# Kernel tuning notes

Hardware: AMD Instinct MI355X
Metric: run time of the kernel (lower is better)

## Reference

```python
import jax, jax.numpy as jnp
import numpy as np

K = 3
IN_C = 64
OUT_C = 64
EMB = 16
N_NODES = 2048
BATCH = 64


def avwgcn(X, E, weights_pool, bias_pool):
    # X: [B, N, C], E: [N, D], weights_pool: [D, K, C, O], bias_pool: [D, O]
    N = E.shape[0]
    A = jax.nn.softmax(jax.nn.relu(E @ E.T), axis=1)  # [N, N]
    supports = [jnp.eye(N, dtype=X.dtype), A]
    for _ in range(2, K):  # Chebyshev recursion
        supports.append(2.0 * (A @ supports[-1]) - supports[-2])
    S = jnp.stack(supports, axis=0)  # [K, N, N]
    W = jnp.einsum('nd,dkio->nkio', E, weights_pool)  # [N, K, C, O]
    b = E @ bias_pool  # [N, O]
    XG = jnp.einsum('knm,bmc->bnkc', S, X)  # [B, N, K, C]
    return jnp.einsum('bnki,nkio->bno', XG, W) + b  # [B, N, O]


def glorot(key, shape):
    fan = shape[-2] + shape[-1]
    std = jnp.sqrt(2.0 / fan)
    return jax.random.normal(key, shape, dtype=jnp.float32) * std


def setup_inputs() -> dict:
    key = jax.random.key(0)
    ks = jax.random.split(key, 6)
    cat_c = IN_C + OUT_C
    return {
        'X': jax.random.normal(ks[0], (BATCH, N_NODES, IN_C), dtype=jnp.float32),
        'E': jax.random.normal(ks[1], (N_NODES, EMB), dtype=jnp.float32),
        'H': jax.random.normal(ks[2], (BATCH, N_NODES, OUT_C), dtype=jnp.float32),
        'gate_weights_pool': glorot(ks[3], (EMB, K, cat_c, 2 * OUT_C)),
        'gate_bias_pool': jnp.zeros((EMB, 2 * OUT_C), dtype=jnp.float32),
        'update_weights_pool': glorot(ks[4], (EMB, K, cat_c, OUT_C)),
        'update_bias_pool': jnp.zeros((EMB, OUT_C), dtype=jnp.float32),
    }


def reference(X, E, H, gate_weights_pool, gate_bias_pool, update_weights_pool, update_bias_pool):
    XH = jnp.concatenate([X, H], axis=-1)  # [B, N, in+out]
    ZR = jax.nn.sigmoid(avwgcn(XH, E, gate_weights_pool, gate_bias_pool))
    Z, R = jnp.split(ZR, 2, axis=-1)
    C = jnp.concatenate([X, Z * H], axis=-1)
    HC = jnp.tanh(avwgcn(C, E, update_weights_pool, update_bias_pool))
    return R * H + (1.0 - R) * HC
```

## Files before the change

kernel.cpp:

```cpp
#include <hip/hip_runtime.h>
#include <hip/hip_fp16.h>


#define B_  64
#define N_  2048
#define D_  16
#define CO_ 64
#define CC_ 128

typedef _Float16 f16x8 __attribute__((ext_vector_type(8)));
typedef float    f32x4 __attribute__((ext_vector_type(4)));

static __device__ __forceinline__ uint pack2(float a, float b) {
  return (uint)__half_as_ushort(__float2half(a)) |
         ((uint)__half_as_ushort(__float2half(b)) << 16);
}

__global__ __launch_bounds__(256)
void k_softmaxA(const float* __restrict__ E, __half* __restrict__ A) {
  const int n = blockIdx.x, t = threadIdx.x;
  __shared__ float row[N_];
  __shared__ float red[4];
  const float4* en4 = reinterpret_cast<const float4*>(E + n * D_);
  const float4 e0 = en4[0], e1 = en4[1], e2 = en4[2], e3 = en4[3];
  float lmax = 0.f;
  for (int m = t; m < N_; m += 256) {
    const float4* em4 = reinterpret_cast<const float4*>(E + m * D_);
    const float4 f0 = em4[0], f1 = em4[1], f2 = em4[2], f3 = em4[3];
    float d = e0.x*f0.x + e0.y*f0.y + e0.z*f0.z + e0.w*f0.w
            + e1.x*f1.x + e1.y*f1.y + e1.z*f1.z + e1.w*f1.w
            + e2.x*f2.x + e2.y*f2.y + e2.z*f2.z + e2.w*f2.w
            + e3.x*f3.x + e3.y*f3.y + e3.z*f3.z + e3.w*f3.w;
    d = fmaxf(d, 0.f);
    row[m] = d;
    lmax = fmaxf(lmax, d);
  }
  #pragma unroll
  for (int off = 32; off > 0; off >>= 1) lmax = fmaxf(lmax, __shfl_down(lmax, off));
  __syncthreads();
  if ((t & 63) == 0) red[t >> 6] = lmax;
  __syncthreads();
  const float gmax = fmaxf(fmaxf(red[0], red[1]), fmaxf(red[2], red[3]));
  float lsum = 0.f;
  for (int m = t; m < N_; m += 256) {
    float v = __expf(row[m] - gmax);
    row[m] = v;
    lsum += v;
  }
  #pragma unroll
  for (int off = 32; off > 0; off >>= 1) lsum += __shfl_down(lsum, off);
  __syncthreads();
  if ((t & 63) == 0) red[t >> 6] = lsum;
  __syncthreads();
  const float rinv = 1.f / (red[0] + red[1] + red[2] + red[3]);
  for (int m = t; m < N_; m += 256)
    A[(long)n * N_ + m] = __float2half(row[m] * rinv);
}

__global__ __launch_bounds__(256)
void k_gemm(const __half* __restrict__ Ag, const __half* __restrict__ Bg,
            __half* __restrict__ Cg, int K, int lda, int ldb, int ldc,
            long sB, long sC) {
  const int m0 = blockIdx.x * 128;
  const int n0 = blockIdx.y * 128;
  Bg += (long)blockIdx.z * sB;
  Cg += (long)blockIdx.z * sC;
  __shared__ __half As[128][40];
  __shared__ __half Bs[128][40];
  const int t = threadIdx.x, lane = t & 63, wid = t >> 6;
  const int wm = (wid & 1) * 64, wn = (wid >> 1) * 64;
  f32x4 acc[4][4] = {};
  const int ar = t >> 1, aseg = t & 1;
  const int bc = t & 127, bkg = (t >> 7) * 8;

  for (int kt = 0; kt < K; kt += 32) {
    {
      const uint4* asrc = reinterpret_cast<const uint4*>(
          Ag + (long)(m0 + ar) * lda + kt + aseg * 16);
      uint4 av0 = asrc[0], av1 = asrc[1];
      *reinterpret_cast<uint4*>(&As[ar][aseg * 16])     = av0;
      *reinterpret_cast<uint4*>(&As[ar][aseg * 16 + 8]) = av1;
    }
    #pragma unroll
    for (int it = 0; it < 2; ++it) {
      const int kk = bkg + it * 16;
      const __half* bsrc = Bg + (long)(kt + kk) * ldb + n0 + bc;
      ushort h[8];
      #pragma unroll
      for (int j = 0; j < 8; ++j) h[j] = __half_as_ushort(bsrc[(long)j * ldb]);
      uint4 pk;
      pk.x = (uint)h[0] | ((uint)h[1] << 16);
      pk.y = (uint)h[2] | ((uint)h[3] << 16);
      pk.z = (uint)h[4] | ((uint)h[5] << 16);
      pk.w = (uint)h[6] | ((uint)h[7] << 16);
      *reinterpret_cast<uint4*>(&Bs[bc][kk]) = pk;
    }
    __syncthreads();
    f16x8 af[4], bf[4];
    #pragma unroll
    for (int i = 0; i < 4; ++i) {
      af[i] = *reinterpret_cast<const f16x8*>(&As[wm + i * 16 + (lane & 15)][(lane >> 4) * 8]);
      bf[i] = *reinterpret_cast<const f16x8*>(&Bs[wn + i * 16 + (lane & 15)][(lane >> 4) * 8]);
    }
    #pragma unroll
    for (int i = 0; i < 4; ++i)
      #pragma unroll
      for (int j = 0; j < 4; ++j)
        acc[i][j] = __builtin_amdgcn_mfma_f32_16x16x32_f16(af[i], bf[j], acc[i][j], 0, 0, 0);
    __syncthreads();
  }
  const int cr = (lane >> 4) * 4, ccol = lane & 15;
  #pragma unroll
  for (int i = 0; i < 4; ++i)
    #pragma unroll
    for (int j = 0; j < 4; ++j) {
      const int gr = m0 + wm + i * 16 + cr;
      const int gc = n0 + wn + j * 16 + ccol;
      #pragma unroll
      for (int r = 0; r < 4; ++r)
        Cg[(long)(gr + r) * ldc + gc] = __float2half(acc[i][j][r]);
    }
}

template <int OSZ>
__global__ __launch_bounds__(256)
void k_wpre(const float* __restrict__ pool, const float* __restrict__ E,
            __half* __restrict__ W, int n0) {
  const int WC = 3 * OSZ * 128;
  const int col0 = blockIdx.x * 512;
  const int kc = col0 / (OSZ * 128);
  const int o0 = (col0 - kc * OSZ * 128) >> 7;
  const int t = threadIdx.x;
  __shared__ float PoolS[16 * 768];
  __shared__ float Es[32][16];
  for (int p = t; p < 512; p += 256)
    Es[p >> 4][p & 15] = E[(n0 + blockIdx.y * 32 + (p >> 4)) * 16 + (p & 15)];
  for (int p = t; p < 16 * 512; p += 256) {
    const int d = p >> 9, jl = p & 511;
    const int o = o0 + (jl >> 7), i = jl & 127;
    PoolS[d * 768 + (jl >> 3) * 12 + (jl & 7)] =
        pool[((long)(d * 3 + kc) * 128 + i) * OSZ + o];
  }
  __syncthreads();
  const int c8 = (t & 63) * 8;
  const int r0 = (t >> 6) * 8;
  const int cbase = (t & 63) * 12;
  float acc[8][8] = {};
  #pragma unroll
  for (int d = 0; d < 16; ++d) {
    const float4 pv0 = *reinterpret_cast<const float4*>(&PoolS[d * 768 + cbase]);
    const float4 pv1 = *reinterpret_cast<const float4*>(&PoolS[d * 768 + cbase + 4]);
    #pragma unroll
    for (int rr = 0; rr < 8; ++rr) {
      const float e = Es[r0 + rr][d];
      acc[rr][0] += e * pv0.x; acc[rr][1] += e * pv0.y;
      acc[rr][2] += e * pv0.z; acc[rr][3] += e * pv0.w;
      acc[rr][4] += e * pv1.x; acc[rr][5] += e * pv1.y;
      acc[rr][6] += e * pv1.z; acc[rr][7] += e * pv1.w;
    }
  }
  #pragma unroll
  for (int rr = 0; rr < 8; ++rr) {
    const int nloc = blockIdx.y * 32 + r0 + rr;
    uint4 pk;
    pk.x = pack2(acc[rr][0], acc[rr][1]);
    pk.y = pack2(acc[rr][2], acc[rr][3]);
    pk.z = pack2(acc[rr][4], acc[rr][5]);
    pk.w = pack2(acc[rr][6], acc[rr][7]);
    *reinterpret_cast<uint4*>(W + (long)nloc * WC + col0 + c8) = pk;
  }
}

__global__ __launch_bounds__(256)
void k_build_xh(const float* __restrict__ X, const float* __restrict__ H,
                __half* __restrict__ XH) {
  const long i = (long)blockIdx.x * 256 + threadIdx.x;
  const long bn = i >> 5;
  const int  q  = (int)(i & 31);
  const float* src = (q < 16 ? X : H) + bn * 64 + (q & 15) * 4;
  const float4 v = *reinterpret_cast<const float4*>(src);
  ushort4 h;
  h.x = __half_as_ushort(__float2half(v.x));
  h.y = __half_as_ushort(__float2half(v.y));
  h.z = __half_as_ushort(__float2half(v.z));
  h.w = __half_as_ushort(__float2half(v.w));
  *reinterpret_cast<ushort4*>(XH + bn * CC_ + q * 4) = h;
}

__global__ __launch_bounds__(256)
void k_cast_f16(const float* __restrict__ src, __half* __restrict__ dst, int nquads) {
  const int i = blockIdx.x * 256 + threadIdx.x;
  if (i >= nquads) return;
  const float4 v = reinterpret_cast<const float4*>(src)[i];
  ushort4 h;
  h.x = __half_as_ushort(__float2half(v.x));
  h.y = __half_as_ushort(__float2half(v.y));
  h.z = __half_as_ushort(__float2half(v.z));
  h.w = __half_as_ushort(__float2half(v.w));
  *reinterpret_cast<ushort4*>(dst + i * 4) = h;
}

__global__ __launch_bounds__(256)
void k_bias(const float* __restrict__ E, const float* __restrict__ pool,
            float* __restrict__ bias, int O) {
  const int idx = blockIdx.x * 256 + threadIdx.x;
  const int n = idx / O, o = idx - n * O;
  float s = 0.f;
  #pragma unroll
  for (int d = 0; d < D_; ++d) s += E[n * D_ + d] * pool[d * O + o];
  bias[idx] = s;
}

static __device__ __forceinline__
void stage_data(int kc, const __half* XH, const __half* G1, const __half* G2,
                long base, int b, int seg, __half (*Ds)[136]) {
  if (kc < 2) {
    const uint4* s = reinterpret_cast<const uint4*>((kc ? G1 : XH) + base);
    uint4 v0 = s[0], v1 = s[1], v2 = s[2], v3 = s[3];
    uint4* d = reinterpret_cast<uint4*>(&Ds[b][seg * 32]);
    d[0] = v0; d[1] = v1; d[2] = v2; d[3] = v3;
  } else {
    const uint4* sg = reinterpret_cast<const uint4*>(G2 + base);
    const uint4* sx = reinterpret_cast<const uint4*>(XH + base);
    #pragma unroll
    for (int q = 0; q < 4; ++q) {
      uint4 g = sg[q], x = sx[q], r;
      const __half2* gh = reinterpret_cast<const __half2*>(&g);
      const __half2* xh = reinterpret_cast<const __half2*>(&x);
      __half2* rh = reinterpret_cast<__half2*>(&r);
      #pragma unroll
      for (int w = 0; w < 4; ++w) rh[w] = __hsub2(__hadd2(gh[w], gh[w]), xh[w]);
      reinterpret_cast<uint4*>(&Ds[b][seg * 32])[q] = r;
    }
  }
}

template <bool PRE>
__global__ __launch_bounds__(256)
void k_gate(const __half* __restrict__ XH, const __half* __restrict__ G1,
            const __half* __restrict__ G2, const __half* __restrict__ Wsrc,
            const float* __restrict__ E, const float* __restrict__ bg,
            const float* __restrict__ H, __half* __restrict__ XHw,
            __half* __restrict__ R, int n0) {
  const int bl = blockIdx.x, n = n0 + bl;
  const int t = threadIdx.x, lane = t & 63, wid = t >> 6;
  __shared__ __half Ws[128][136];
  __shared__ __half Ds[64][136];
  __shared__ float es[D_];
  if constexpr (!PRE) {
    if (t < D_) es[t] = E[n * D_ + t];
    __syncthreads();
  }
  f32x4 acc[4][2] = {};
  #pragma unroll
  for (int kc = 0; kc < 3; ++kc) {
    {
      const int b = t & 63, seg = t >> 6;
      stage_data(kc, XH, G1, G2, ((long)b * N_ + n) * CC_ + seg * 32, b, seg, Ds);
    }
    if constexpr (PRE) {
      const uint4* s4 = reinterpret_cast<const uint4*>(
          Wsrc + ((long)(bl * 3 + kc) * 128 + (t >> 1)) * 128 + (t & 1) * 64);
      uint4* dst = reinterpret_cast<uint4*>(&Ws[t >> 1][(t & 1) * 64]);
      #pragma unroll
      for (int q = 0; q < 8; ++q) dst[q] = s4[q];
    } else {
      const __half* pk = Wsrc + (long)kc * 128 * 128;
      for (int p = t; p < 64 * 128; p += 256) {
        const int o2 = p & 63, i = p >> 6;
        float w0 = 0.f, w1 = 0.f;
        #pragma unroll
        for (int d = 0; d < D_; ++d) {
          const __half2 h2 = *reinterpret_cast<const __half2*>(
              pk + (long)d * 3 * 128 * 128 + i * 128 + o2 * 2);
          const float e = es[d];
          w0 += e * __half2float(h2.x);
          w1 += e * __half2float(h2.y);
        }
        Ws[o2 * 2][i]     = __float2half(w0);
        Ws[o2 * 2 + 1][i] = __float2half(w1);
      }
    }
    __syncthreads();
    #pragma unroll
    for (int ks = 0; ks < 4; ++ks) {
      f16x8 a[4], bf[2];
      #pragma unroll
      for (int i = 0; i < 4; ++i)
        a[i] = *reinterpret_cast<const f16x8*>(&Ds[i * 16 + (lane & 15)][ks * 32 + (lane >> 4) * 8]);
      #pragma unroll
      for (int j = 0; j < 2; ++j)
        bf[j] = *reinterpret_cast<const f16x8*>(&Ws[wid * 32 + j * 16 + (lane & 15)][ks * 32 + (lane >> 4) * 8]);
      #pragma unroll
      for (int i = 0; i < 4; ++i)
        #pragma unroll
        for (int j = 0; j < 2; ++j)
          acc[i][j] = __builtin_amdgcn_mfma_f32_16x16x32_f16(a[i], bf[j], acc[i][j], 0, 0, 0);
    }
    __syncthreads();
  }
  const int cr = (lane >> 4) * 4, co = lane & 15;
  #pragma unroll
  for (int i = 0; i < 4; ++i)
    #pragma unroll
    for (int j = 0; j < 2; ++j) {
      const int o = wid * 32 + j * 16 + co;
      const float bv = bg[n * 128 + o];
      #pragma unroll
      for (int r = 0; r < 4; ++r) {
        const int b = i * 16 + cr + r;
        const float v = acc[i][j][r] + bv;
        const float s = 1.f / (1.f + __expf(-v));
        const long base = ((long)b * N_ + n) * CO_ + (o & 63);
        if (o < 64) {
          XHw[((long)b * N_ + n) * CC_ + 64 + o] = __float2half(s * H[base]);
        } else {
          R[base] = __float2half(s);
        }
      }
    }
}

template <bool PRE>
__global__ __launch_bounds__(256)
void k_update(const __half* __restrict__ C, const __half* __restrict__ G1,
              const __half* __restrict__ G2, const __half* __restrict__ Wsrc,
              const float* __restrict__ E, const float* __restrict__ bu,
              const float* __restrict__ H, const __half* __restrict__ R,
              float* __restrict__ out, int n0) {
  const int bl = blockIdx.x, n = n0 + bl;
  const int t = threadIdx.x, lane = t & 63, wid = t >> 6;
  __shared__ __half Ws[64][136];
  __shared__ __half Ds[64][136];
  __shared__ float es[D_];
  if constexpr (!PRE) {
    if (t < D_) es[t] = E[n * D_ + t];
    __syncthreads();
  }
  f32x4 acc[4] = {};
  #pragma unroll
  for (int kc = 0; kc < 3; ++kc) {
    {
      const int b = t & 63, seg = t >> 6;
      stage_data(kc, C, G1, G2, ((long)b * N_ + n) * CC_ + seg * 32, b, seg, Ds);
    }
    if constexpr (PRE) {
      const uint4* s4 = reinterpret_cast<const uint4*>(
          Wsrc + ((long)(bl * 3 + kc) * 64 + (t >> 2)) * 128 + (t & 3) * 32);
      uint4* dst = reinterpret_cast<uint4*>(&Ws[t >> 2][(t & 3) * 32]);
      #pragma unroll
      for (int q = 0; q < 4; ++q) dst[q] = s4[q];
    } else {
      const __half* pk = Wsrc + (long)kc * 128 * 64;
      for (int p = t; p < 32 * 128; p += 256) {
        const int o2 = p & 31, i = p >> 5;
        float w0 = 0.f, w1 = 0.f;
        #pragma unroll
        for (int d = 0; d < D_; ++d) {
          const __half2 h2 = *reinterpret_cast<const __half2*>(
              pk + (long)d * 3 * 128 * 64 + i * 64 + o2 * 2);
          const float e = es[d];
          w0 += e * __half2float(h2.x);
          w1 += e * __half2float(h2.y);
        }
        Ws[o2 * 2][i]     = __float2half(w0);
        Ws[o2 * 2 + 1][i] = __float2half(w1);
      }
    }
    __syncthreads();
    #pragma unroll
    for (int ks = 0; ks < 4; ++ks) {
      f16x8 a[4], bf;
      #pragma unroll
      for (int i = 0; i < 4; ++i)
        a[i] = *reinterpret_cast<const f16x8*>(&Ds[i * 16 + (lane & 15)][ks * 32 + (lane >> 4) * 8]);
      bf = *reinterpret_cast<const f16x8*>(&Ws[wid * 16 + (lane & 15)][ks * 32 + (lane >> 4) * 8]);
      #pragma unroll
      for (int i = 0; i < 4; ++i)
        acc[i] = __builtin_amdgcn_mfma_f32_16x16x32_f16(a[i], bf, acc[i], 0, 0, 0);
    }
    __syncthreads();
  }
  const int cr = (lane >> 4) * 4, co = lane & 15;
  const int o = wid * 16 + co;
  const float bv = bu[n * 64 + o];
  #pragma unroll
  for (int i = 0; i < 4; ++i)
    #pragma unroll
    for (int r = 0; r < 4; ++r) {
      const int b = i * 16 + cr + r;
      const long idx = ((long)b * N_ + n) * CO_ + o;
      const float hc = tanhf(acc[i][r] + bv);
      const float rr = __half2float(R[idx]);
      out[idx] = rr * H[idx] + (1.f - rr) * hc;
    }
}

extern "C" void kernel_launch(void* const* d_in, const int* in_sizes, int n_in,
                              void* d_out, int out_size, void* d_ws, size_t ws_size,
                              hipStream_t stream) {
  const float* X  = (const float*)d_in[0];
  const float* E  = (const float*)d_in[1];
  const float* H  = (const float*)d_in[2];
  const float* gp = (const float*)d_in[3];
  const float* gb = (const float*)d_in[4];
  const float* up = (const float*)d_in[5];
  const float* ub = (const float*)d_in[6];
  float* out = (float*)d_out;

  size_t off = 0;
  auto alloc = [&](size_t bytes) {
    void* p = (char*)d_ws + off;
    off += (bytes + 255) & ~(size_t)255;
    return p;
  };
  __half* A16  = (__half*)alloc((size_t)N_ * N_ * 2);
  __half* XH   = (__half*)alloc((size_t)B_ * N_ * CC_ * 2);
  __half* G1   = (__half*)alloc((size_t)B_ * N_ * CC_ * 2);
  __half* G2   = (__half*)alloc((size_t)B_ * N_ * CC_ * 2);
  __half* Rb   = (__half*)alloc((size_t)B_ * N_ * CO_ * 2);
  float*  bg   = (float*)alloc((size_t)N_ * 128 * 4);
  float*  bu   = (float*)alloc((size_t)N_ * 64 * 4);

  __half* Wbuf = (__half*)((char*)d_ws + off);
  const size_t rem = (ws_size > off) ? ws_size - off : 0;
  long cgl = (long)(rem / 98304) & ~31L;
  long cul = (long)(rem / 49152) & ~31L;
  const int cg = (int)(cgl > N_ ? N_ : cgl);
  const int cu = (int)(cul > N_ ? N_ : cul);
  const bool pre = cg >= 32;

  const long sXH = (long)N_ * CC_;

  k_bias<<<1024, 256, 0, stream>>>(E, gb, bg, 128);
  k_bias<<<512, 256, 0, stream>>>(E, ub, bu, 64);
  k_softmaxA<<<N_, 256, 0, stream>>>(E, A16);
  k_build_xh<<<16384, 256, 0, stream>>>(X, H, XH);

  k_gemm<<<dim3(16, 1, B_), 256, 0, stream>>>(A16, XH, G1, N_, N_, CC_, CC_, sXH, sXH);
  k_gemm<<<dim3(16, 1, B_), 256, 0, stream>>>(A16, G1, G2, N_, N_, CC_, CC_, sXH, sXH);

  __half* pg = nullptr;
  __half* pu = nullptr;
  if (pre) {
    for (int n0 = 0; n0 < N_; n0 += cg) {
      const int cnt = (N_ - n0 < cg) ? N_ - n0 : cg;
      k_wpre<128><<<dim3(96, cnt / 32), 256, 0, stream>>>(gp, E, Wbuf, n0);
      k_gate<true><<<cnt, 256, 0, stream>>>(XH, G1, G2, Wbuf, E, bg, H, XH, Rb, n0);
    }
  } else {
    pg = (__half*)alloc((size_t)D_ * 3 * 128 * 128 * 2);
    pu = (__half*)alloc((size_t)D_ * 3 * 128 * 64 * 2);
    k_cast_f16<<<768, 256, 0, stream>>>(gp, pg, 196608);
    k_cast_f16<<<384, 256, 0, stream>>>(up, pu, 98304);
    k_gate<false><<<N_, 256, 0, stream>>>(XH, G1, G2, pg, E, bg, H, XH, Rb, 0);
  }

  k_gemm<<<dim3(16, 1, B_), 256, 0, stream>>>(A16, XH, G1, N_, N_, CC_, CC_, sXH, sXH);
  k_gemm<<<dim3(16, 1, B_), 256, 0, stream>>>(A16, G1, G2, N_, N_, CC_, CC_, sXH, sXH);

  if (pre) {
    for (int n0 = 0; n0 < N_; n0 += cu) {
      const int cnt = (N_ - n0 < cu) ? N_ - n0 : cu;
      k_wpre<64><<<dim3(48, cnt / 32), 256, 0, stream>>>(up, E, Wbuf, n0);
      k_update<true><<<cnt, 256, 0, stream>>>(XH, G1, G2, Wbuf, E, bu, H, Rb, out, n0);
    }
  } else {
    k_update<false><<<N_, 256, 0, stream>>>(XH, G1, G2, pu, E, bu, H, Rb, out, 0);
  }
}
```

Baseline: 1.014 ms.

## Rewrite support GEMM with direct global-to-LDS loads, XOR-swizzled tiles, K=64 steps

Replaces the generic fp16 GEMM used for the four A×X support products with a specialized kernel. The A tile is loaded straight into LDS via global_load_lds, and the B tile is read as 16-byte vectors and transposed into an XOR-swizzled LDS layout. Each K step grows from 32 to 64, which halves the number of barriers. The aim is to cut LDS bank conflicts, the scalar strided B loads, and sync overhead. In exchange, dimensions are hardcoded (N_, CC_) and the kernel relies on a low-level builtin.

```diff
diff --git a/kernel.cpp b/kernel.cpp
--- a/kernel.cpp
+++ b/kernel.cpp
@@ -10,6 +10,12 @@
 
 typedef _Float16 f16x8 __attribute__((ext_vector_type(8)));
 typedef float    f32x4 __attribute__((ext_vector_type(4)));
+typedef unsigned short u16x8 __attribute__((ext_vector_type(8)));
+
+#define GLOAD_LDS16(g, l)                                          \
+  __builtin_amdgcn_global_load_lds(                                \
+      (const __attribute__((address_space(1))) unsigned int*)(g),  \
+      (__attribute__((address_space(3))) unsigned int*)(l), 16, 0, 0)
 
 static __device__ __forceinline__ uint pack2(float a, float b) {
   return (uint)__half_as_ushort(__float2half(a)) |
@@ -58,67 +64,81 @@
 }
 
 __global__ __launch_bounds__(256)
-void k_gemm(const __half* __restrict__ Ag, const __half* __restrict__ Bg,
-            __half* __restrict__ Cg, int K, int lda, int ldb, int ldc,
-            long sB, long sC) {
+void k_gemm2(const __half* __restrict__ Ag, const __half* __restrict__ Bg,
+             __half* __restrict__ Cg, long sB, long sC) {
   const int m0 = blockIdx.x * 128;
-  const int n0 = blockIdx.y * 128;
   Bg += (long)blockIdx.z * sB;
   Cg += (long)blockIdx.z * sC;
-  __shared__ __half As[128][40];
-  __shared__ __half Bs[128][40];
+  __shared__ __half As[128 * 64];
+  __shared__ __half Bs[128 * 64];
   const int t = threadIdx.x, lane = t & 63, wid = t >> 6;
   const int wm = (wid & 1) * 64, wn = (wid >> 1) * 64;
+  const int l15 = lane & 15, lq = lane >> 4;
   f32x4 acc[4][4] = {};
-  const int ar = t >> 1, aseg = t & 1;
-  const int bc = t & 127, bkg = (t >> 7) * 8;
-
-  for (int kt = 0; kt < K; kt += 32) {
+
+  const int arow_l = lane >> 3;
+  const int aslot  = lane & 7;
+  const int agran  = aslot ^ arow_l;
+
+  const int jt = t & 15, kg = t >> 4;
+  const int c0 = jt * 8, k0 = kg * 4;
+  const int g4 = kg >> 1, khalf = kg & 1;
+
+  for (int kt = 0; kt < N_; kt += 64) {
+    #pragma unroll
+    for (int i = 0; i < 4; ++i) {
+      const int row8 = (wid * 4 + i) * 8;
+      const __half* src = Ag + (long)(m0 + row8 + arow_l) * N_ + kt + agran * 8;
+      GLOAD_LDS16(src, As + row8 * 64);
+    }
     {
-      const uint4* asrc = reinterpret_cast<const uint4*>(
-          Ag + (long)(m0 + ar) * lda + kt + aseg * 16);
-      uint4 av0 = asrc[0], av1 = asrc[1];
-      *reinterpret_cast<uint4*>(&As[ar][aseg * 16])     = av0;
-      *reinterpret_cast<uint4*>(&As[ar][aseg * 16 + 8]) = av1;
-    }
-    #pragma unroll
-    for (int it = 0; it < 2; ++it) {
-      const int kk = bkg + it * 16;
-      const __half* bsrc = Bg + (long)(kt + kk) * ldb + n0 + bc;
-      ushort h[8];
-      #pragma unroll
-      for (int j = 0; j < 8; ++j) h[j] = __half_as_ushort(bsrc[(long)j * ldb]);
-      uint4 pk;
-      pk.x = (uint)h[0] | ((uint)h[1] << 16);
-      pk.y = (uint)h[2] | ((uint)h[3] << 16);
-      pk.z = (uint)h[4] | ((uint)h[5] << 16);
-      pk.w = (uint)h[6] | ((uint)h[7] << 16);
-      *reinterpret_cast<uint4*>(&Bs[bc][kk]) = pk;
-    }
-    __syncthreads();
-    f16x8 af[4], bf[4];
-    #pragma unroll
-    for (int i = 0; i < 4; ++i) {
-      af[i] = *reinterpret_cast<const f16x8*>(&As[wm + i * 16 + (lane & 15)][(lane >> 4) * 8]);
-      bf[i] = *reinterpret_cast<const f16x8*>(&Bs[wn + i * 16 + (lane & 15)][(lane >> 4) * 8]);
-    }
-    #pragma unroll
-    for (int i = 0; i < 4; ++i)
-      #pragma unroll
-      for (int j = 0; j < 4; ++j)
-        acc[i][j] = __builtin_amdgcn_mfma_f32_16x16x32_f16(af[i], bf[j], acc[i][j], 0, 0, 0);
-    __syncthreads();
-  }
-  const int cr = (lane >> 4) * 4, ccol = lane & 15;
+      u16x8 bv[4];
+      #pragma unroll
+      for (int r = 0; r < 4; ++r)
+        bv[r] = *reinterpret_cast<const u16x8*>(Bg + (long)(kt + k0 + r) * CC_ + c0);
+      #pragma unroll
+      for (int jc = 0; jc < 8; ++jc) {
+        const int j = c0 + jc;
+        const int s = ((j >> 3) & 7) ^ (j & 7);
+        ushort4 w;
+        w.x = bv[0][jc]; w.y = bv[1][jc]; w.z = bv[2][jc]; w.w = bv[3][jc];
+        *reinterpret_cast<ushort4*>(Bs + j * 64 + ((g4 ^ s) << 3) + (khalf << 2)) = w;
+      }
+    }
+    __syncthreads();
+    #pragma unroll
+    for (int kh = 0; kh < 2; ++kh) {
+      const int gr = kh * 4 + lq;
+      f16x8 af[4], bf[4];
+      #pragma unroll
+      for (int i = 0; i < 4; ++i) {
+        const int row = wm + i * 16 + l15;
+        af[i] = *reinterpret_cast<const f16x8*>(As + row * 64 + ((gr ^ (row & 7)) << 3));
+      }
+      #pragma unroll
+      for (int j = 0; j < 4; ++j) {
+        const int col = wn + j * 16 + l15;
+        const int s = ((col >> 3) & 7) ^ (col & 7);
+        bf[j] = *reinterpret_cast<const f16x8*>(Bs + col * 64 + ((gr ^ s) << 3));
+      }
+      #pragma unroll
+      for (int i = 0; i < 4; ++i)
+        #pragma unroll
+        for (int j = 0; j < 4; ++j)
+          acc[i][j] = __builtin_amdgcn_mfma_f32_16x16x32_f16(af[i], bf[j], acc[i][j], 0, 0, 0);
+    }
+    __syncthreads();
+  }
+  const int cr = lq * 4, ccol = l15;
   #pragma unroll
   for (int i = 0; i < 4; ++i)
     #pragma unroll
     for (int j = 0; j < 4; ++j) {
-      const int gr = m0 + wm + i * 16 + cr;
-      const int gc = n0 + wn + j * 16 + ccol;
+      const int grow = m0 + wm + i * 16 + cr;
+      const int gcol = wn + j * 16 + ccol;
       #pragma unroll
       for (int r = 0; r < 4; ++r)
-        Cg[(long)(gr + r) * ldc + gc] = __float2half(acc[i][j][r]);
+        Cg[(long)(grow + r) * CC_ + gcol] = __float2half(acc[i][j][r]);
     }
 }
 
@@ -437,8 +457,8 @@
   k_softmaxA<<<N_, 256, 0, stream>>>(E, A16);
   k_build_xh<<<16384, 256, 0, stream>>>(X, H, XH);
 
-  k_gemm<<<dim3(16, 1, B_), 256, 0, stream>>>(A16, XH, G1, N_, N_, CC_, CC_, sXH, sXH);
-  k_gemm<<<dim3(16, 1, B_), 256, 0, stream>>>(A16, G1, G2, N_, N_, CC_, CC_, sXH, sXH);
+  k_gemm2<<<dim3(16, 1, B_), 256, 0, stream>>>(A16, XH, G1, sXH, sXH);
+  k_gemm2<<<dim3(16, 1, B_), 256, 0, stream>>>(A16, G1, G2, sXH, sXH);
 
   __half* pg = nullptr;
   __half* pu = nullptr;
@@ -456,8 +476,8 @@
     k_gate<false><<<N_, 256, 0, stream>>>(XH, G1, G2, pg, E, bg, H, XH, Rb, 0);
   }
 
-  k_gemm<<<dim3(16, 1, B_), 256, 0, stream>>>(A16, XH, G1, N_, N_, CC_, CC_, sXH, sXH);
-  k_gemm<<<dim3(16, 1, B_), 256, 0, stream>>>(A16, G1, G2, N_, N_, CC_, CC_, sXH, sXH);
+  k_gemm2<<<dim3(16, 1, B_), 256, 0, stream>>>(A16, XH, G1, sXH, sXH);
+  k_gemm2<<<dim3(16, 1, B_), 256, 0, stream>>>(A16, G1, G2, sXH, sXH);
 
   if (pre) {
     for (int n0 = 0; n0 < N_; n0 += cu) {
```

Result: faster. 910.3 us (-10.2%).
